# Optimization experiments

Hardware: AMD Instinct MI355X
Metric: run time of the kernel (lower is better)

## Reference

```python
import jax, jax.numpy as jnp
import numpy as np

B, IN, OUT = 131072, 512, 512


def setup_inputs() -> dict:
    key = jax.random.key(0)
    k1, k2 = jax.random.split(key)
    x = jax.random.normal(k1, (B, IN), dtype=jnp.float32)
    # matches reset_parameters: normal(0, sqrt(1/in_features))
    weight = jax.random.normal(k2, (OUT, IN), dtype=jnp.float32) * jnp.sqrt(1.0 / IN)
    bias = jnp.zeros((OUT,), dtype=jnp.float32)
    return {"x": x, "weight": weight, "bias": bias}


def _binarize(w):
    # deterministic sign binarization: w >= 0 -> +1, else -1
    return jnp.where(w >= 0, 1.0, -1.0).astype(w.dtype)


def reference(x, weight, bias):
    wb = _binarize(weight)            # [out, in], values in {-1, +1}
    # out = x @ wb.T + bias           # [B, out]
    return jnp.einsum("bi,oi->bo", x, wb) + bias
```

## Files before the change

### kernel.cpp

```cpp
#include <hip/hip_runtime.h>
#include <stdint.h>


#define BATCH   131072
#define IN_F    512
#define OUT_F   512
#define BM      64
#define NKT     32

using f32x4  = __attribute__((ext_vector_type(4))) float;
using f32x16 = __attribute__((ext_vector_type(16))) float;
using short8 = __attribute__((ext_vector_type(8))) short;
using usv8   = __attribute__((ext_vector_type(8))) unsigned short;
using u32    = uint32_t;

__global__ void prep_w(const float* __restrict__ W, unsigned short* __restrict__ wf) {
    int t = blockIdx.x * blockDim.x + threadIdx.x;
    int l  = t & 63;
    int nf = (t >> 6) & 15;
    int kt = t >> 10;
    int n = nf * 32 + (l & 31);
    int k = kt * 16 + ((l >> 5) << 3);
    const float* src = W + (size_t)n * IN_F + k;
    f32x4 w0 = *(const f32x4*)(src);
    f32x4 w1 = *(const f32x4*)(src + 4);
    usv8 o;
#pragma unroll
    for (int j = 0; j < 4; ++j) {
        o[j]     = (w0[j] >= 0.0f) ? 0x3F80u : 0xBF80u;
        o[j + 4] = (w1[j] >= 0.0f) ? 0x3F80u : 0xBF80u;
    }
    *(usv8*)(wf + (size_t)t * 8) = o;
}

__global__ __launch_bounds__(512, 4) void gemm_bin(
    const float* __restrict__ X, const unsigned short* __restrict__ WF,
    const float* __restrict__ bias, float* __restrict__ out) {

    __shared__ __align__(16) unsigned short lds[BM * IN_F];

    const int tid  = threadIdx.x;
    const int lane = tid & 63;
    const int wv   = tid >> 6;
    const int m0   = blockIdx.x * BM;

    {
        const int r  = tid >> 3;
        const int sg = tid & 7;
        const float* xr = X + (size_t)(m0 + r) * IN_F;
        char* lrow = (char*)lds + r * 1024;
        const int swz = (r & 7) << 4;
#pragma unroll
        for (int p = 0; p < 8; ++p) {
            const int f0 = sg * 8 + p * 64;
            f32x4 a = *(const f32x4*)(xr + f0);
            f32x4 b = *(const f32x4*)(xr + f0 + 4);
            u32 w0, w1, w2, w3;
            asm("v_cvt_pk_bf16_f32 %0, %1, %2" : "=v"(w0) : "v"(a[0]), "v"(a[1]));
            asm("v_cvt_pk_bf16_f32 %0, %1, %2" : "=v"(w1) : "v"(a[2]), "v"(a[3]));
            asm("v_cvt_pk_bf16_f32 %0, %1, %2" : "=v"(w2) : "v"(b[0]), "v"(b[1]));
            asm("v_cvt_pk_bf16_f32 %0, %1, %2" : "=v"(w3) : "v"(b[2]), "v"(b[3]));
            union { u32 w[4]; usv8 v; } pk;
            pk.w[0] = w0; pk.w[1] = w1; pk.w[2] = w2; pk.w[3] = w3;
            *(usv8*)(lrow + ((sg * 16 + p * 128) ^ swz)) = pk.v;
        }
    }

    f32x16 acc[2][2];
#pragma unroll
    for (int fn = 0; fn < 2; ++fn) {
        const float bv = bias[wv * 64 + fn * 32 + (lane & 31)];
#pragma unroll
        for (int rg = 0; rg < 2; ++rg)
#pragma unroll
            for (int r = 0; r < 16; ++r) acc[rg][fn][r] = bv;
    }
    __syncthreads();

    const int arow  = (lane & 31) * 1024;
    const int ak4   = (lane >> 5) << 4;
    const int aswz  = (lane & 7) << 4;
    const char* lptr = (const char*)lds;
    const short8* wb = (const short8*)(WF) + ((size_t)(wv * 2) * 64 + lane);

#define LDA(dst, kt_)                                                          \
    {                                                                          \
        const int koff_ = ((kt_) * 32 + ak4) ^ aswz;                           \
        _Pragma("unroll")                                                      \
        for (int rg = 0; rg < 2; ++rg)                                         \
            dst[rg] = *(const short8*)(lptr + rg * 32768 + arow + koff_);      \
    }
#define LDB(dst, kt_)                                                          \
    {                                                                          \
        _Pragma("unroll")                                                      \
        for (int fn = 0; fn < 2; ++fn)                                         \
            dst[fn] = wb[(kt_) * 1024 + fn * 64];                              \
    }

    short8 af[2][2], bf[2][2];
    LDA(af[0], 0);
    LDB(bf[0], 0);

#pragma unroll
    for (int kt = 0; kt < NKT; ++kt) {
        const int cur = kt & 1;
        if (kt < NKT - 1) {
            LDB(bf[cur ^ 1], kt + 1);
            LDA(af[cur ^ 1], kt + 1);
        }
#pragma unroll
        for (int rg = 0; rg < 2; ++rg)
#pragma unroll
            for (int fn = 0; fn < 2; ++fn)
                acc[rg][fn] = __builtin_amdgcn_mfma_f32_32x32x16_bf16(
                    af[cur][rg], bf[cur][fn], acc[rg][fn], 0, 0, 0);
    }
#undef LDA
#undef LDB

    const int c     = lane & 31;
    const int rbase = (lane >> 5) << 2;
#pragma unroll
    for (int rg = 0; rg < 2; ++rg)
#pragma unroll
        for (int fn = 0; fn < 2; ++fn)
#pragma unroll
            for (int r = 0; r < 16; ++r) {
                const int row = rg * 32 + (r & 3) + 8 * (r >> 2) + rbase;
                out[(size_t)(m0 + row) * OUT_F + wv * 64 + fn * 32 + c] =
                    acc[rg][fn][r];
            }
}

extern "C" void kernel_launch(void* const* d_in, const int* in_sizes, int n_in,
                              void* d_out, int out_size, void* d_ws, size_t ws_size,
                              hipStream_t stream) {
    const float* X    = (const float*)d_in[0];
    const float* W    = (const float*)d_in[1];
    const float* bias = (const float*)d_in[2];
    float* o          = (float*)d_out;
    unsigned short* wf = (unsigned short*)d_ws;

    hipLaunchKernelGGL(prep_w, dim3(128), dim3(256), 0, stream, W, wf);
    hipLaunchKernelGGL(gemm_bin, dim3(BATCH / BM), dim3(512), 0, stream,
                       X, wf, bias, o);
}
```

Measured before the change: 138.7 us.

## Make GEMM blocks persistent over eight row tiles with double-buffered LDS staging

Each block now runs eight consecutive 64-row tiles instead of one, with the grid cut to 256 blocks. The next tile's X rows are loaded into registers during the current tile's MFMA loop, then converted to bf16 into a second LDS buffer. This hides global-load latency behind compute and overlaps the store epilogue. It doubles LDS use and adds 64 staging registers per thread, so occupancy drops to 2 blocks per CU, and the B fragments are prefetched two k-steps ahead.

```diff
diff --git a/kernel.cpp b/kernel.cpp
--- a/kernel.cpp
+++ b/kernel.cpp
@@ -7,6 +7,8 @@
 #define OUT_F   512
 #define BM      64
 #define NKT     32
+#define NS      8
+#define GRID    256
 
 using f32x4  = __attribute__((ext_vector_type(4))) float;
 using f32x16 = __attribute__((ext_vector_type(16))) float;
@@ -33,63 +35,80 @@
     *(usv8*)(wf + (size_t)t * 8) = o;
 }
 
-__global__ __launch_bounds__(512, 4) void gemm_bin(
+__global__ __launch_bounds__(512, 2) void gemm_bin(
     const float* __restrict__ X, const unsigned short* __restrict__ WF,
     const float* __restrict__ bias, float* __restrict__ out) {
 
-    __shared__ __align__(16) unsigned short lds[BM * IN_F];
+    __shared__ __align__(16) char smem[2 * BM * IN_F * 2];
 
     const int tid  = threadIdx.x;
     const int lane = tid & 63;
     const int wv   = tid >> 6;
-    const int m0   = blockIdx.x * BM;
+    const size_t row0 = (size_t)blockIdx.x * (NS * BM);
 
-    {
-        const int r  = tid >> 3;
-        const int sg = tid & 7;
-        const float* xr = X + (size_t)(m0 + r) * IN_F;
-        char* lrow = (char*)lds + r * 1024;
-        const int swz = (r & 7) << 4;
-#pragma unroll
-        for (int p = 0; p < 8; ++p) {
-            const int f0 = sg * 8 + p * 64;
-            f32x4 a = *(const f32x4*)(xr + f0);
-            f32x4 b = *(const f32x4*)(xr + f0 + 4);
-            u32 w0, w1, w2, w3;
-            asm("v_cvt_pk_bf16_f32 %0, %1, %2" : "=v"(w0) : "v"(a[0]), "v"(a[1]));
-            asm("v_cvt_pk_bf16_f32 %0, %1, %2" : "=v"(w1) : "v"(a[2]), "v"(a[3]));
-            asm("v_cvt_pk_bf16_f32 %0, %1, %2" : "=v"(w2) : "v"(b[0]), "v"(b[1]));
-            asm("v_cvt_pk_bf16_f32 %0, %1, %2" : "=v"(w3) : "v"(b[2]), "v"(b[3]));
-            union { u32 w[4]; usv8 v; } pk;
-            pk.w[0] = w0; pk.w[1] = w1; pk.w[2] = w2; pk.w[3] = w3;
-            *(usv8*)(lrow + ((sg * 16 + p * 128) ^ swz)) = pk.v;
-        }
+    const int sr   = tid >> 3;
+    const int sg   = tid & 7;
+    const int sswz = (sr & 7) << 4;
+    const float* xbase = X + (row0 + sr) * IN_F + sg * 8;
+
+    const int arow = (lane & 31) * 1024;
+    const int ak4  = (lane >> 5) << 4;
+    const int aswz = (lane & 7) << 4;
+
+    const short8* wb = (const short8*)WF + ((size_t)(wv * 2) * 64 + lane);
+
+    const float bv0 = bias[wv * 64 + (lane & 31)];
+    const float bv1 = bias[wv * 64 + 32 + (lane & 31)];
+
+    f32x4  stg[16];
+    f32x16 acc[2][2];
+
+#define STG_LOAD(s_)                                                           \
+    {                                                                          \
+        const float* xr_ = xbase + (size_t)(s_) * (BM * IN_F);                 \
+        _Pragma("unroll")                                                      \
+        for (int p = 0; p < 8; ++p) {                                          \
+            stg[2 * p]     = *(const f32x4*)(xr_ + p * 64);                    \
+            stg[2 * p + 1] = *(const f32x4*)(xr_ + p * 64 + 4);                \
+        }                                                                      \
     }
 
-    f32x16 acc[2][2];
-#pragma unroll
-    for (int fn = 0; fn < 2; ++fn) {
-        const float bv = bias[wv * 64 + fn * 32 + (lane & 31)];
-#pragma unroll
-        for (int rg = 0; rg < 2; ++rg)
-#pragma unroll
-            for (int r = 0; r < 16; ++r) acc[rg][fn][r] = bv;
+#define STG_WRITE(b_)                                                          \
+    {                                                                          \
+        char* lrow_ = smem + (b_) * 65536 + sr * 1024;                         \
+        _Pragma("unroll")                                                      \
+        for (int p = 0; p < 8; ++p) {                                          \
+            u32 w0, w1, w2, w3;                                                \
+            asm("v_cvt_pk_bf16_f32 %0, %1, %2" : "=v"(w0)                      \
+                : "v"(stg[2*p][0]), "v"(stg[2*p][1]));                         \
+            asm("v_cvt_pk_bf16_f32 %0, %1, %2" : "=v"(w1)                      \
+                : "v"(stg[2*p][2]), "v"(stg[2*p][3]));                         \
+            asm("v_cvt_pk_bf16_f32 %0, %1, %2" : "=v"(w2)                      \
+                : "v"(stg[2*p+1][0]), "v"(stg[2*p+1][1]));                     \
+            asm("v_cvt_pk_bf16_f32 %0, %1, %2" : "=v"(w3)                      \
+                : "v"(stg[2*p+1][2]), "v"(stg[2*p+1][3]));                     \
+            union { u32 w[4]; usv8 v; } pk_;                                   \
+            pk_.w[0] = w0; pk_.w[1] = w1; pk_.w[2] = w2; pk_.w[3] = w3;        \
+            *(usv8*)(lrow_ + ((sg * 16 + p * 128) ^ sswz)) = pk_.v;            \
+        }                                                                      \
     }
-    __syncthreads();
 
-    const int arow  = (lane & 31) * 1024;
-    const int ak4   = (lane >> 5) << 4;
-    const int aswz  = (lane & 7) << 4;
-    const char* lptr = (const char*)lds;
-    const short8* wb = (const short8*)(WF) + ((size_t)(wv * 2) * 64 + lane);
+#define ACC_INIT                                                               \
+    {                                                                          \
+        _Pragma("unroll")                                                      \
+        for (int r_ = 0; r_ < 16; ++r_) {                                      \
+            acc[0][0][r_] = bv0; acc[0][1][r_] = bv1;                          \
+            acc[1][0][r_] = bv0; acc[1][1][r_] = bv1;                          \
+        }                                                                      \
+    }
 
 #define LDA(dst, kt_)                                                          \
     {                                                                          \
-        const int koff_ = ((kt_) * 32 + ak4) ^ aswz;                           \
-        _Pragma("unroll")                                                      \
-        for (int rg = 0; rg < 2; ++rg)                                         \
-            dst[rg] = *(const short8*)(lptr + rg * 32768 + arow + koff_);      \
+        const int ko_ = (((kt_) * 32) + ak4) ^ aswz;                           \
+        dst[0] = *(const short8*)(lptr + arow + ko_);                          \
+        dst[1] = *(const short8*)(lptr + 32768 + arow + ko_);                  \
     }
+
 #define LDB(dst, kt_)                                                          \
     {                                                                          \
         _Pragma("unroll")                                                      \
@@ -97,39 +116,58 @@
             dst[fn] = wb[(kt_) * 1024 + fn * 64];                              \
     }
 
-    short8 af[2][2], bf[2][2];
-    LDA(af[0], 0);
-    LDB(bf[0], 0);
+    STG_LOAD(0);
+    STG_WRITE(0);
+    ACC_INIT;
+    __syncthreads();
 
+#pragma unroll 1
+    for (int s = 0; s < NS; ++s) {
+        const int cb = s & 1;
+        if (s + 1 < NS) STG_LOAD(s + 1);
+
+        const char* lptr = smem + cb * 65536;
+        short8 af[2][2], bf[4][2];
+        LDA(af[0], 0);
+        LDB(bf[0], 0);
+        LDB(bf[1], 1);
 #pragma unroll
-    for (int kt = 0; kt < NKT; ++kt) {
-        const int cur = kt & 1;
-        if (kt < NKT - 1) {
-            LDB(bf[cur ^ 1], kt + 1);
-            LDA(af[cur ^ 1], kt + 1);
+        for (int kt = 0; kt < NKT; ++kt) {
+            if (kt + 1 < NKT) LDA(af[(kt + 1) & 1], kt + 1);
+            if (kt + 2 < NKT) LDB(bf[(kt + 2) & 3], kt + 2);
+#pragma unroll
+            for (int rg = 0; rg < 2; ++rg)
+#pragma unroll
+                for (int fn = 0; fn < 2; ++fn)
+                    acc[rg][fn] = __builtin_amdgcn_mfma_f32_32x32x16_bf16(
+                        af[kt & 1][rg], bf[kt & 3][fn], acc[rg][fn], 0, 0, 0);
         }
+
+        if (s + 1 < NS) STG_WRITE(cb ^ 1);
+
+        {
+            const size_t m0 = row0 + (size_t)s * BM;
+            const int c     = lane & 31;
+            const int rbase = (lane >> 5) << 2;
 #pragma unroll
-        for (int rg = 0; rg < 2; ++rg)
+            for (int rg = 0; rg < 2; ++rg)
 #pragma unroll
-            for (int fn = 0; fn < 2; ++fn)
-                acc[rg][fn] = __builtin_amdgcn_mfma_f32_32x32x16_bf16(
-                    af[cur][rg], bf[cur][fn], acc[rg][fn], 0, 0, 0);
+                for (int fn = 0; fn < 2; ++fn)
+#pragma unroll
+                    for (int r_ = 0; r_ < 16; ++r_) {
+                        const int row = rg * 32 + (r_ & 3) + 8 * (r_ >> 2) + rbase;
+                        out[(m0 + row) * OUT_F + wv * 64 + fn * 32 + c] =
+                            acc[rg][fn][r_];
+                    }
+        }
+        ACC_INIT;
+        __syncthreads();
     }
+#undef STG_LOAD
+#undef STG_WRITE
+#undef ACC_INIT
 #undef LDA
 #undef LDB
-
-    const int c     = lane & 31;
-    const int rbase = (lane >> 5) << 2;
-#pragma unroll
-    for (int rg = 0; rg < 2; ++rg)
-#pragma unroll
-        for (int fn = 0; fn < 2; ++fn)
-#pragma unroll
-            for (int r = 0; r < 16; ++r) {
-                const int row = rg * 32 + (r & 3) + 8 * (r >> 2) + rbase;
-                out[(size_t)(m0 + row) * OUT_F + wv * 64 + fn * 32 + c] =
-                    acc[rg][fn][r];
-            }
 }
 
 extern "C" void kernel_launch(void* const* d_in, const int* in_sizes, int n_in,
@@ -142,6 +180,6 @@
     unsigned short* wf = (unsigned short*)d_ws;
 
     hipLaunchKernelGGL(prep_w, dim3(128), dim3(256), 0, stream, W, wf);
-    hipLaunchKernelGGL(gemm_bin, dim3(BATCH / BM), dim3(512), 0, stream,
+    hipLaunchKernelGGL(gemm_bin, dim3(GRID), dim3(512), 0, stream,
                        X, wf, bias, o);
 }
```

Result: slower. 326.5 us (+135.5%).

## Stream X tiles into LDS via async global_load_lds with multi-buffered pipeline

Applied to the files above, without the earlier changes.

Replaces the upfront synchronous load-convert-store of the whole X tile into LDS with a 4-buffer ring of 64-column fp32 chunks fetched by global_load_lds DMA, issued two chunks ahead. The bf16 conversion moves to after the LDS read, just before the MFMA. Manual vmcnt waits and barriers order the stages, so global latency can overlap compute instead of stalling before the main loop. LDS holds fp32, which doubles the read traffic and adds conversion work in the inner loop. The vmcnt counting is fragile because it must also cover the interleaved B loads.

```diff
diff --git a/kernel.cpp b/kernel.cpp
--- a/kernel.cpp
+++ b/kernel.cpp
@@ -6,7 +6,8 @@
 #define IN_F    512
 #define OUT_F   512
 #define BM      64
-#define NKT     32
+#define NCH     8
+#define BUFB    16384
 
 using f32x4  = __attribute__((ext_vector_type(4))) float;
 using f32x16 = __attribute__((ext_vector_type(16))) float;
@@ -33,37 +34,70 @@
     *(usv8*)(wf + (size_t)t * 8) = o;
 }
 
+__device__ __forceinline__ void wait_vm6() { asm volatile("s_waitcnt vmcnt(6)" ::: "memory"); }
+__device__ __forceinline__ void wait_vm4() { asm volatile("s_waitcnt vmcnt(4)" ::: "memory"); }
+
 __global__ __launch_bounds__(512, 4) void gemm_bin(
     const float* __restrict__ X, const unsigned short* __restrict__ WF,
     const float* __restrict__ bias, float* __restrict__ out) {
 
-    __shared__ __align__(16) unsigned short lds[BM * IN_F];
+    __shared__ __align__(16) char smem[4 * BUFB];
 
     const int tid  = threadIdx.x;
     const int lane = tid & 63;
     const int wv   = tid >> 6;
     const int m0   = blockIdx.x * BM;
 
-    {
-        const int r  = tid >> 3;
-        const int sg = tid & 7;
-        const float* xr = X + (size_t)(m0 + r) * IN_F;
-        char* lrow = (char*)lds + r * 1024;
-        const int swz = (r & 7) << 4;
-#pragma unroll
-        for (int p = 0; p < 8; ++p) {
-            const int f0 = sg * 8 + p * 64;
-            f32x4 a = *(const f32x4*)(xr + f0);
-            f32x4 b = *(const f32x4*)(xr + f0 + 4);
-            u32 w0, w1, w2, w3;
-            asm("v_cvt_pk_bf16_f32 %0, %1, %2" : "=v"(w0) : "v"(a[0]), "v"(a[1]));
-            asm("v_cvt_pk_bf16_f32 %0, %1, %2" : "=v"(w1) : "v"(a[2]), "v"(a[3]));
-            asm("v_cvt_pk_bf16_f32 %0, %1, %2" : "=v"(w2) : "v"(b[0]), "v"(b[1]));
-            asm("v_cvt_pk_bf16_f32 %0, %1, %2" : "=v"(w3) : "v"(b[2]), "v"(b[3]));
-            union { u32 w[4]; usv8 v; } pk;
-            pk.w[0] = w0; pk.w[1] = w1; pk.w[2] = w2; pk.w[3] = w3;
-            *(usv8*)(lrow + ((sg * 16 + p * 128) ^ swz)) = pk.v;
-        }
+    const int dr   = wv * 4 + (lane >> 4);
+    const int dc   = (lane & 15) * 16;
+    const int dswz = (dr & 7) << 4;
+    const float* src0 = X + (size_t)(m0 + dr) * IN_F + ((dc ^ dswz) >> 2);
+    const float* src1 = src0 + (size_t)32 * IN_F;
+
+#define ISSUE_DMA(ck_)                                                         \
+    {                                                                          \
+        char* b_ = smem + ((ck_) & 3) * BUFB + wv * 1024;                      \
+        __builtin_amdgcn_global_load_lds(                                      \
+            (const __attribute__((address_space(1))) void*)(src0 + (ck_) * 64),\
+            (__attribute__((address_space(3))) void*)(b_), 16, 0, 0);          \
+        __builtin_amdgcn_global_load_lds(                                      \
+            (const __attribute__((address_space(1))) void*)(src1 + (ck_) * 64),\
+            (__attribute__((address_space(3))) void*)(b_ + 8192), 16, 0, 0);   \
+    }
+
+    const short8* wb = (const short8*)(WF) + ((size_t)(wv * 2) * 64 + lane);
+#define LDB(dst, g_)                                                           \
+    {                                                                          \
+        _Pragma("unroll")                                                      \
+        for (int fn = 0; fn < 2; ++fn)                                         \
+            dst[fn] = wb[(g_) * 1024 + fn * 64];                               \
+    }
+
+    const int arow = (lane & 31) * 256;
+    const int aq32 = (lane >> 5) << 5;
+    const int aswz = (lane & 7) << 4;
+
+#define LDA_CVT(dst, ab_, kt4_)                                                \
+    {                                                                          \
+        _Pragma("unroll")                                                      \
+        for (int rg = 0; rg < 2; ++rg) {                                       \
+            const char* p_  = (ab_) + rg * 8192 + arow;                        \
+            const int  blo_ = (((kt4_) << 6) + aq32) ^ aswz;                   \
+            f32x4 lo_ = *(const f32x4*)(p_ + blo_);                            \
+            f32x4 hi_ = *(const f32x4*)(p_ + (blo_ ^ 16));                     \
+            u32 w0_, w1_, w2_, w3_;                                            \
+            asm("v_cvt_pk_bf16_f32 %0, %1, %2" : "=v"(w0_)                     \
+                : "v"(lo_[0]), "v"(lo_[1]));                                   \
+            asm("v_cvt_pk_bf16_f32 %0, %1, %2" : "=v"(w1_)                     \
+                : "v"(lo_[2]), "v"(lo_[3]));                                   \
+            asm("v_cvt_pk_bf16_f32 %0, %1, %2" : "=v"(w2_)                     \
+                : "v"(hi_[0]), "v"(hi_[1]));                                   \
+            asm("v_cvt_pk_bf16_f32 %0, %1, %2" : "=v"(w3_)                     \
+                : "v"(hi_[2]), "v"(hi_[3]));                                   \
+            union { u32 w[4]; short8 v; } pk_;                                 \
+            pk_.w[0] = w0_; pk_.w[1] = w1_; pk_.w[2] = w2_; pk_.w[3] = w3_;    \
+            dst[rg] = pk_.v;                                                   \
+        }                                                                      \
     }
 
     f32x16 acc[2][2];
@@ -75,48 +109,39 @@
 #pragma unroll
             for (int r = 0; r < 16; ++r) acc[rg][fn][r] = bv;
     }
-    __syncthreads();
 
-    const int arow  = (lane & 31) * 1024;
-    const int ak4   = (lane >> 5) << 4;
-    const int aswz  = (lane & 7) << 4;
-    const char* lptr = (const char*)lds;
-    const short8* wb = (const short8*)(WF) + ((size_t)(wv * 2) * 64 + lane);
+    ISSUE_DMA(0);
+    ISSUE_DMA(1);
 
-#define LDA(dst, kt_)                                                          \
-    {                                                                          \
-        const int koff_ = ((kt_) * 32 + ak4) ^ aswz;                           \
-        _Pragma("unroll")                                                      \
-        for (int rg = 0; rg < 2; ++rg)                                         \
-            dst[rg] = *(const short8*)(lptr + rg * 32768 + arow + koff_);      \
+    short8 bf[2][2];
+#pragma unroll
+    for (int ck = 0; ck < NCH; ++ck) {
+        LDB(bf[0], ck * 4 + 0);
+        LDB(bf[1], ck * 4 + 1);
+        __builtin_amdgcn_sched_barrier(0);
+        if (ck < NCH - 1) wait_vm6(); else wait_vm4();
+        __builtin_amdgcn_sched_barrier(0);
+        __builtin_amdgcn_s_barrier();
+        __builtin_amdgcn_sched_barrier(0);
+        if (ck + 2 < NCH) ISSUE_DMA(ck + 2);
+
+        const char* ab = smem + (ck & 3) * BUFB;
+        short8 af[2];
+#pragma unroll
+        for (int kt4 = 0; kt4 < 4; ++kt4) {
+            LDA_CVT(af, ab, kt4);
+#pragma unroll
+            for (int rg = 0; rg < 2; ++rg)
+#pragma unroll
+                for (int fn = 0; fn < 2; ++fn)
+                    acc[rg][fn] = __builtin_amdgcn_mfma_f32_32x32x16_bf16(
+                        af[rg], bf[kt4 & 1][fn], acc[rg][fn], 0, 0, 0);
+            if (kt4 < 2) LDB(bf[kt4 & 1], ck * 4 + kt4 + 2);
+        }
     }
-#define LDB(dst, kt_)                                                          \
-    {                                                                          \
-        _Pragma("unroll")                                                      \
-        for (int fn = 0; fn < 2; ++fn)                                         \
-            dst[fn] = wb[(kt_) * 1024 + fn * 64];                              \
-    }
-
-    short8 af[2][2], bf[2][2];
-    LDA(af[0], 0);
-    LDB(bf[0], 0);
-
-#pragma unroll
-    for (int kt = 0; kt < NKT; ++kt) {
-        const int cur = kt & 1;
-        if (kt < NKT - 1) {
-            LDB(bf[cur ^ 1], kt + 1);
-            LDA(af[cur ^ 1], kt + 1);
-        }
-#pragma unroll
-        for (int rg = 0; rg < 2; ++rg)
-#pragma unroll
-            for (int fn = 0; fn < 2; ++fn)
-                acc[rg][fn] = __builtin_amdgcn_mfma_f32_32x32x16_bf16(
-                    af[cur][rg], bf[cur][fn], acc[rg][fn], 0, 0, 0);
-    }
-#undef LDA
+#undef ISSUE_DMA
 #undef LDB
+#undef LDA_CVT
 
     const int c     = lane & 31;
     const int rbase = (lane >> 5) << 2;
```

New measurement: 136.7 us. About the same (-1.4%).

## Double the row tile to 128 and use a 2x4 wave grid with deeper B prefetch

Applied to the files above, without the earlier changes.

Raises the block tile to 128 rows, arranging the 8 waves as 2x4 so each wave computes a 64x128 output tile and reuses each A fragment across four B fragments. The binarized weight fragments are now prefetched two k-steps ahead, with s_setprio raised around the MFMA cluster. The aim is fewer weight reads per output and fewer LDS reads per MFMA. In exchange, LDS use doubles to 128KB, so only one block fits per CU, and register pressure rises, which lowers occupancy and latency hiding for a kernel dominated by memory traffic.

```diff
diff --git a/kernel.cpp b/kernel.cpp
--- a/kernel.cpp
+++ b/kernel.cpp
@@ -5,7 +5,7 @@
 #define BATCH   131072
 #define IN_F    512
 #define OUT_F   512
-#define BM      64
+#define BM      128
 #define NKT     32
 
 using f32x4  = __attribute__((ext_vector_type(4))) float;
@@ -33,7 +33,7 @@
     *(usv8*)(wf + (size_t)t * 8) = o;
 }
 
-__global__ __launch_bounds__(512, 4) void gemm_bin(
+__global__ __launch_bounds__(512, 2) void gemm_bin(
     const float* __restrict__ X, const unsigned short* __restrict__ WF,
     const float* __restrict__ bias, float* __restrict__ out) {
 
@@ -42,19 +42,20 @@
     const int tid  = threadIdx.x;
     const int lane = tid & 63;
     const int wv   = tid >> 6;
+    const int wm   = wv >> 2;
+    const int wn   = wv & 3;
     const int m0   = blockIdx.x * BM;
 
     {
-        const int r  = tid >> 3;
-        const int sg = tid & 7;
-        const float* xr = X + (size_t)(m0 + r) * IN_F;
+        const int r  = tid >> 2;
+        const int sg = tid & 3;
+        const float* xr = X + (size_t)(m0 + r) * IN_F + sg * 128;
         char* lrow = (char*)lds + r * 1024;
-        const int swz = (r & 7) << 4;
+        const int msk = (r & 15) << 4;
 #pragma unroll
-        for (int p = 0; p < 8; ++p) {
-            const int f0 = sg * 8 + p * 64;
-            f32x4 a = *(const f32x4*)(xr + f0);
-            f32x4 b = *(const f32x4*)(xr + f0 + 4);
+        for (int p = 0; p < 16; ++p) {
+            f32x4 a = *(const f32x4*)(xr + p * 8);
+            f32x4 b = *(const f32x4*)(xr + p * 8 + 4);
             u32 w0, w1, w2, w3;
             asm("v_cvt_pk_bf16_f32 %0, %1, %2" : "=v"(w0) : "v"(a[0]), "v"(a[1]));
             asm("v_cvt_pk_bf16_f32 %0, %1, %2" : "=v"(w1) : "v"(a[2]), "v"(a[3]));
@@ -62,14 +63,14 @@
             asm("v_cvt_pk_bf16_f32 %0, %1, %2" : "=v"(w3) : "v"(b[2]), "v"(b[3]));
             union { u32 w[4]; usv8 v; } pk;
             pk.w[0] = w0; pk.w[1] = w1; pk.w[2] = w2; pk.w[3] = w3;
-            *(usv8*)(lrow + ((sg * 16 + p * 128) ^ swz)) = pk.v;
+            *(usv8*)(lrow + ((sg * 256 + p * 16) ^ msk)) = pk.v;
         }
     }
 
-    f32x16 acc[2][2];
+    f32x16 acc[2][4];
 #pragma unroll
-    for (int fn = 0; fn < 2; ++fn) {
-        const float bv = bias[wv * 64 + fn * 32 + (lane & 31)];
+    for (int fn = 0; fn < 4; ++fn) {
+        const float bv = bias[wn * 128 + fn * 32 + (lane & 31)];
 #pragma unroll
         for (int rg = 0; rg < 2; ++rg)
 #pragma unroll
@@ -77,43 +78,44 @@
     }
     __syncthreads();
 
-    const int arow  = (lane & 31) * 1024;
+    const int arow  = (wm * 64 + (lane & 31)) * 1024;
     const int ak4   = (lane >> 5) << 4;
-    const int aswz  = (lane & 7) << 4;
+    const int aswz  = (lane & 15) << 4;
     const char* lptr = (const char*)lds;
-    const short8* wb = (const short8*)(WF) + ((size_t)(wv * 2) * 64 + lane);
 
 #define LDA(dst, kt_)                                                          \
     {                                                                          \
         const int koff_ = ((kt_) * 32 + ak4) ^ aswz;                           \
-        _Pragma("unroll")                                                      \
-        for (int rg = 0; rg < 2; ++rg)                                         \
-            dst[rg] = *(const short8*)(lptr + rg * 32768 + arow + koff_);      \
+        dst[0] = *(const short8*)(lptr + arow + koff_);                        \
+        dst[1] = *(const short8*)(lptr + arow + 32768 + koff_);                \
     }
+
+    const short8* wb = (const short8*)(WF) + ((size_t)(wn * 4) * 64 + lane);
 #define LDB(dst, kt_)                                                          \
     {                                                                          \
         _Pragma("unroll")                                                      \
-        for (int fn = 0; fn < 2; ++fn)                                         \
+        for (int fn = 0; fn < 4; ++fn)                                         \
             dst[fn] = wb[(kt_) * 1024 + fn * 64];                              \
     }
 
-    short8 af[2][2], bf[2][2];
+    short8 af[2][2], bf[2][4];
     LDA(af[0], 0);
     LDB(bf[0], 0);
+    LDB(bf[1], 1);
 
 #pragma unroll
     for (int kt = 0; kt < NKT; ++kt) {
         const int cur = kt & 1;
-        if (kt < NKT - 1) {
-            LDB(bf[cur ^ 1], kt + 1);
-            LDA(af[cur ^ 1], kt + 1);
-        }
+        if (kt < NKT - 1) LDA(af[cur ^ 1], kt + 1);
+        __builtin_amdgcn_s_setprio(1);
 #pragma unroll
         for (int rg = 0; rg < 2; ++rg)
 #pragma unroll
-            for (int fn = 0; fn < 2; ++fn)
+            for (int fn = 0; fn < 4; ++fn)
                 acc[rg][fn] = __builtin_amdgcn_mfma_f32_32x32x16_bf16(
                     af[cur][rg], bf[cur][fn], acc[rg][fn], 0, 0, 0);
+        __builtin_amdgcn_s_setprio(0);
+        if (kt < NKT - 2) LDB(bf[cur], kt + 2);
     }
 #undef LDA
 #undef LDB
@@ -123,11 +125,11 @@
 #pragma unroll
     for (int rg = 0; rg < 2; ++rg)
 #pragma unroll
-        for (int fn = 0; fn < 2; ++fn)
+        for (int fn = 0; fn < 4; ++fn)
 #pragma unroll
             for (int r = 0; r < 16; ++r) {
-                const int row = rg * 32 + (r & 3) + 8 * (r >> 2) + rbase;
-                out[(size_t)(m0 + row) * OUT_F + wv * 64 + fn * 32 + c] =
+                const int row = wm * 64 + rg * 32 + (r & 3) + 8 * (r >> 2) + rbase;
+                out[(size_t)(m0 + row) * OUT_F + wn * 128 + fn * 32 + c] =
                     acc[rg][fn][r];
             }
 }
```

After: 149.5 us. +7.8%, slower.
